# Performance work log

Hardware: AMD Instinct MI355X
Metric: run time of the kernel (lower is better)

The kernel has to match this reference:

```python
import jax, jax.numpy as jnp
import numpy as np

N = 4096   # nodes
E = 4096   # hyperedges (== N so the original's [N,H] output is fully populated)
F = 256    # feature_size
H = 256    # hidden_size
BLOCK = 64 # node-block size for the blocked masked max/min scan


def setup_inputs() -> dict:
    key = jax.random.key(0)
    ks = jax.random.split(key, 11)
    mask = jax.random.randint(ks[4], (E, N), 0, 2, dtype=jnp.int32)
    # guarantee every hyperedge is non-empty (matches `if end > start` path)
    mask = mask.at[jnp.arange(E), jnp.arange(N)].set(1)
    s = 0.05
    return {
        "pos_features": jax.random.normal(ks[0], (N, F), jnp.float32),
        "pos_matrix": jax.random.normal(ks[1], (N, F), jnp.float32),
        "neg_features": jax.random.normal(ks[2], (N, F), jnp.float32),
        "neg_matrix": jax.random.normal(ks[3], (N, F), jnp.float32),
        "batch_mask": mask,
        "W_self": jax.random.normal(ks[5], (F, H), jnp.float32) * s,
        "b_self": jnp.zeros((H,), jnp.float32),
        "W_hyper": jax.random.normal(ks[6], (F, H), jnp.float32) * s,
        "b_hyper": jnp.zeros((H,), jnp.float32),
        "W_score": jax.random.normal(ks[7], (H, 1), jnp.float32) * s,
        "b_score": jnp.zeros((1,), jnp.float32),
    }


def maxmin_pool(mask_bool, feats):
    """Per-hyperedge (max - min) over member-node features.
    mask_bool: [E, N] bool, feats: [N, H] -> [E, H].
    Blocked over nodes to avoid materializing [E, N, H]."""
    Ee, Nn = mask_bool.shape
    Hh = feats.shape[1]
    nb = Nn // BLOCK
    mask_blocks = mask_bool.reshape(Ee, nb, BLOCK).transpose(1, 0, 2)  # [nb, E, BLOCK]
    feat_blocks = feats.reshape(nb, BLOCK, Hh)                          # [nb, BLOCK, H]

    def body(carry, xs):
        mx, mn = carry
        mblk, fblk = xs                      # [E, BLOCK], [BLOCK, H]
        m = mblk[:, :, None]                 # [E, BLOCK, 1]
        f = fblk[None]                       # [1, BLOCK, H]
        mx = jnp.maximum(mx, jnp.max(jnp.where(m, f, -jnp.inf), axis=1))
        mn = jnp.minimum(mn, jnp.min(jnp.where(m, f, jnp.inf), axis=1))
        return (mx, mn), None

    init = (jnp.full((Ee, Hh), -jnp.inf, feats.dtype),
            jnp.full((Ee, Hh), jnp.inf, feats.dtype))
    (mx, mn), _ = jax.lax.scan(body, init, (mask_blocks, feat_blocks))
    return mx - mn


def reference(pos_features, pos_matrix, neg_features, neg_matrix, batch_mask,
              W_self, b_self, W_hyper, b_hyper, W_score, b_score):
    mask = batch_mask.astype(bool)

    def branch(x_feat, x_mat):
        h = jax.nn.relu(x_feat @ W_self + b_self + x_mat @ W_hyper + b_hyper)  # [N, H]
        pooled = maxmin_pool(mask, h)                                          # [E, H]
        return jax.nn.sigmoid(pooled @ W_score + b_score)                      # [E, 1]

    pos_score = branch(pos_features, pos_matrix)
    neg_score = branch(neg_features, neg_matrix)
    return pos_score, neg_score
```

## Files before the change

kernel.cpp:

```cpp
#include <hip/hip_runtime.h>
#include <hip/hip_bf16.h>
#include <hip/hip_fp16.h>


typedef short bf16x8 __attribute__((ext_vector_type(8)));
typedef float f32x4 __attribute__((ext_vector_type(4)));
typedef short s16x2 __attribute__((ext_vector_type(2)));
typedef unsigned short u16x2 __attribute__((ext_vector_type(2)));

static __device__ __forceinline__ unsigned short f2bf(float f) {
    __hip_bfloat16 b = __float2bfloat16(f);
    return __builtin_bit_cast(unsigned short, b);
}
static __device__ __forceinline__ float f16u_to_f(unsigned u) {
    __half h = __builtin_bit_cast(__half, (unsigned short)(u & 0xffffu));
    return __half2float(h);
}
static __device__ __forceinline__ unsigned pkmax_i16(unsigned a, unsigned b) {
    s16x2 r = __builtin_elementwise_max(__builtin_bit_cast(s16x2, a), __builtin_bit_cast(s16x2, b));
    return __builtin_bit_cast(unsigned, r);
}
static __device__ __forceinline__ unsigned pkmin_u16(unsigned a, unsigned b) {
    u16x2 r = __builtin_elementwise_min(__builtin_bit_cast(u16x2, a), __builtin_bit_cast(u16x2, b));
    return __builtin_bit_cast(unsigned, r);
}

__global__ void k_prepW(const float* __restrict__ Ws, const float* __restrict__ Wh,
                        unsigned short* __restrict__ Wts, unsigned short* __restrict__ Wth) {
    __shared__ unsigned short tile[64][65];
    const int k0 = blockIdx.x * 64, n0 = blockIdx.y * 64;
    const float* W     = blockIdx.z ? Wh : Ws;
    unsigned short* Wt = blockIdx.z ? Wth : Wts;
    const int t = threadIdx.x;
#pragma unroll
    for (int m = 0; m < 16; m++) {
        int li = t + m * 256; int r = li >> 6, c = li & 63;
        tile[r][c] = f2bf(W[(size_t)(k0 + r) * 256 + n0 + c]);
    }
    __syncthreads();
#pragma unroll
    for (int m = 0; m < 16; m++) {
        int li = t + m * 256; int c2 = li >> 6, r2 = li & 63;
        Wt[(size_t)(n0 + c2) * 256 + k0 + r2] = tile[r2][c2];
    }
}

__global__ void k_pack(const int* __restrict__ mask, unsigned* __restrict__ packed) {
    const int w = blockIdx.x * 256 + threadIdx.x;
    const int* p = mask + (size_t)w * 32;
    unsigned word = 0;
#pragma unroll
    for (int j = 0; j < 32; j += 4) {
        int4 m = *(const int4*)(p + j);
        word |= (m.x != 0 ? (1u << (31 - j)) : 0u)
              | (m.y != 0 ? (1u << (30 - j)) : 0u)
              | (m.z != 0 ? (1u << (29 - j)) : 0u)
              | (m.w != 0 ? (1u << (28 - j)) : 0u);
    }
    packed[w] = word;
}

__launch_bounds__(256)
__global__ void k_gemm_relu(const float* __restrict__ pXf, const float* __restrict__ pXm,
                            const float* __restrict__ nXf, const float* __restrict__ nXm,
                            const unsigned short* __restrict__ Wts, const unsigned short* __restrict__ Wth,
                            const float* __restrict__ bs,  const float* __restrict__ bh,
                            unsigned short* __restrict__ hOut, int tmode) {
    const int t  = threadIdx.x;
    const int wv = t >> 6;
    const int l  = t & 63;
    const int lm = l & 15;
    const int q  = l >> 4;
    const int bz = blockIdx.z;
    const float* Xf = bz ? nXf : pXf;
    const float* Xm = bz ? nXm : pXm;
    unsigned short* hb = hOut + (size_t)bz * 4096 * 256;

    const int m0 = blockIdx.x * 64 + wv * 16;
    const int n0 = blockIdx.y * 64;

    f32x4 acc[4] = {};
#pragma unroll
    for (int ks = 0; ks < 512; ks += 32) {
        const float* X           = (ks < 256) ? Xf : Xm;
        const unsigned short* Wt = (ks < 256) ? Wts : Wth;
        const int kk = (ks & 255) + q * 8;
        float4 a0 = *(const float4*)(X + (m0 + lm) * 256 + kk);
        float4 a1 = *(const float4*)(X + (m0 + lm) * 256 + kk + 4);
        bf16x8 a;
        a[0] = (short)f2bf(a0.x); a[1] = (short)f2bf(a0.y);
        a[2] = (short)f2bf(a0.z); a[3] = (short)f2bf(a0.w);
        a[4] = (short)f2bf(a1.x); a[5] = (short)f2bf(a1.y);
        a[6] = (short)f2bf(a1.z); a[7] = (short)f2bf(a1.w);
#pragma unroll
        for (int nt = 0; nt < 4; nt++) {
            bf16x8 b = *(const bf16x8*)(Wt + (n0 + nt * 16 + lm) * 256 + kk);
            acc[nt] = __builtin_amdgcn_mfma_f32_16x16x32_bf16(a, b, acc[nt], 0, 0, 0);
        }
    }
    if (tmode) {
#pragma unroll
        for (int nt = 0; nt < 4; nt++) {
            const int c = n0 + nt * 16 + lm;
            const float bsum = bs[c] + bh[c];
            ushort4 v4;
#pragma unroll
            for (int i = 0; i < 4; i++) {
                float v = acc[nt][i] + bsum;
                v = v > 0.f ? v : 0.f;
                ((unsigned short*)&v4)[i] = __builtin_bit_cast(unsigned short, __float2half(v));
            }
            *(ushort4*)(hb + (size_t)c * 4096 + m0 + q * 4) = v4;
        }
    } else {
#pragma unroll
        for (int nt = 0; nt < 4; nt++) {
            const int c = n0 + nt * 16 + lm;
            const float bsum = bs[c] + bh[c];
#pragma unroll
            for (int i = 0; i < 4; i++) {
                const int r = m0 + q * 4 + i;
                float v = acc[nt][i] + bsum;
                v = v > 0.f ? v : 0.f;
                hb[(size_t)r * 256 + c] = __builtin_bit_cast(unsigned short, __float2half(v));
            }
        }
    }
}

__launch_bounds__(256)
__global__ void k_sortpack(const unsigned short* __restrict__ hT,
                           const int* __restrict__ mask,
                           unsigned* __restrict__ packed,
                           unsigned* __restrict__ topkG, unsigned* __restrict__ botkG) {
    __shared__ unsigned arrA[4096];
    __shared__ unsigned arrB[4096];
    __shared__ unsigned short hist[16 * 256];

    const int c = blockIdx.x, br = blockIdx.y, t = threadIdx.x;
    const int wv = t >> 6, l = t & 63;
    const unsigned short* src = hT + (size_t)(br * 256 + c) * 4096;

    const int gtid = (br * 256 + c) * 256 + t;
    const int4* mp = (const int4*)(mask + (size_t)gtid * 128);
    int4 mr[16];
#pragma unroll
    for (int i = 0; i < 16; i++) mr[i] = mp[i];

    {
        uint4 a = ((const uint4*)src)[t * 2];
        uint4 b = ((const uint4*)src)[t * 2 + 1];
        unsigned base = t * 16;
        unsigned w[8] = {a.x, a.y, a.z, a.w, b.x, b.y, b.z, b.w};
#pragma unroll
        for (int m = 0; m < 8; m++) {
            arrA[base + 2 * m]     = ((w[m] & 0xFFFFu) << 16) | (base + 2 * m);
            arrA[base + 2 * m + 1] = (w[m] & 0xFFFF0000u)     | (base + 2 * m + 1);
        }
    }
    __syncthreads();

    unsigned pw[4];
#pragma unroll
    for (int m = 0; m < 2; m++) {
        unsigned word = 0;
#pragma unroll
        for (int j2 = 0; j2 < 8; j2++) {
            int4 v = mr[m * 8 + j2];
            const int j = j2 * 4;
            word |= (v.x != 0 ? (1u << (31 - j)) : 0u)
                  | (v.y != 0 ? (1u << (30 - j)) : 0u)
                  | (v.z != 0 ? (1u << (29 - j)) : 0u)
                  | (v.w != 0 ? (1u << (28 - j)) : 0u);
        }
        pw[m] = word;
    }
#pragma unroll
    for (int i = 0; i < 16; i++) mr[i] = mp[16 + i];

    unsigned* A = arrA;
    unsigned* B = arrB;
    auto do_pass = [&](int sh) {
        unsigned keys[16];
        unsigned short cnt[16];
#pragma unroll
        for (int b = 0; b < 16; b++) cnt[b] = 0;
#pragma unroll
        for (int m = 0; m < 16; m++) {
            keys[m] = A[t * 16 + m];
            cnt[(keys[m] >> sh) & 15u]++;
        }
#pragma unroll
        for (int b = 0; b < 16; b++) hist[b * 256 + t] = cnt[b];
        __syncthreads();

        unsigned loc[16];
        unsigned sum = 0;
#pragma unroll
        for (int m = 0; m < 16; m++) { loc[m] = sum; sum += hist[t * 16 + m]; }
        unsigned ws = sum;
#pragma unroll
        for (int off = 1; off < 64; off <<= 1) {
            unsigned n = __shfl_up(ws, off);
            if (l >= off) ws += n;
        }
        if (l == 63) B[wv] = ws;
        __syncthreads();
        unsigned wbase = 0;
#pragma unroll
        for (int w2 = 0; w2 < 4; w2++) if (w2 < wv) wbase += B[w2];
        const unsigned ex = wbase + ws - sum;
#pragma unroll
        for (int m = 0; m < 16; m++) hist[t * 16 + m] = (unsigned short)(ex + loc[m]);
        __syncthreads();

        unsigned offs[16];
#pragma unroll
        for (int b = 0; b < 16; b++) offs[b] = hist[b * 256 + t];
#pragma unroll
        for (int m = 0; m < 16; m++) {
            unsigned b = (keys[m] >> sh) & 15u;
            B[offs[b]++] = keys[m];
        }
        __syncthreads();
        unsigned* tmp = A; A = B; B = tmp;
    };

    do_pass(16);
#pragma unroll
    for (int m = 0; m < 2; m++) {
        unsigned word = 0;
#pragma unroll
        for (int j2 = 0; j2 < 8; j2++) {
            int4 v = mr[m * 8 + j2];
            const int j = j2 * 4;
            word |= (v.x != 0 ? (1u << (31 - j)) : 0u)
                  | (v.y != 0 ? (1u << (30 - j)) : 0u)
                  | (v.z != 0 ? (1u << (29 - j)) : 0u)
                  | (v.w != 0 ? (1u << (28 - j)) : 0u);
        }
        pw[2 + m] = word;
    }
    do_pass(20);
    do_pass(24);
    do_pass(28);

    if (t < 64) {
        topkG[(br * 64 + t) * 256 + c] = arrA[4095 - t];
        botkG[(br * 64 + t) * 256 + c] = arrA[t];
    }
    *(uint4*)(packed + (size_t)gtid * 4) = make_uint4(pw[0], pw[1], pw[2], pw[3]);
}

__launch_bounds__(256)
__global__ void k_probe(const unsigned* __restrict__ topkG,
                        const unsigned* __restrict__ botkG,
                        const unsigned* __restrict__ packed,
                        const unsigned short* __restrict__ hT,
                        const float* __restrict__ Wscore,
                        const float* __restrict__ bscore,
                        float* __restrict__ out) {
    __shared__ __align__(16) unsigned topkL[16 * 256];
    __shared__ __align__(16) unsigned botkL[16 * 256];
    __shared__ __align__(16) unsigned bitsL[16 * 128];

    const int t  = threadIdx.x;
    const int wv = t >> 6;
    const int l  = t & 63;
    const int e0 = blockIdx.x * 16;
    const int br = blockIdx.y;

    {
        const uint4* ts  = (const uint4*)(topkG + br * 16384);
        const uint4* bs2 = (const uint4*)(botkG + br * 16384);
#pragma unroll
        for (int m = 0; m < 4; m++) {
            ((uint4*)topkL)[t + m * 256] = ts[t + m * 256];
            ((uint4*)botkL)[t + m * 256] = bs2[t + m * 256];
        }
        ((uint4*)bitsL)[t]       = ((const uint4*)(packed + e0 * 128))[t];
        ((uint4*)bitsL)[t + 256] = ((const uint4*)(packed + e0 * 128))[t + 256];
    }
    __syncthreads();

    const float bsc = *bscore;
    float wsv[4];
#pragma unroll
    for (int sl = 0; sl < 4; sl++) wsv[sl] = Wscore[l + 64 * sl];

#pragma unroll 1
    for (int k = 0; k < 4; k++) {
        const int e = wv * 4 + k;
        const unsigned* mk = &bitsL[e * 128];
        float s = 0.f;
#pragma unroll
        for (int sl = 0; sl < 4; sl++) {
            const int c = l + 64 * sl;

            unsigned sel = 0xFFFFFFFFu;
#pragma unroll 1
            for (int g = 0; g < 2; g++) {
                unsigned kk[8]; int ss[8];
#pragma unroll
                for (int j = 0; j < 8; j++) kk[j] = topkL[(g * 8 + j) * 256 + c];
#pragma unroll
                for (int j = 0; j < 8; j++)
                    ss[j] = (int)(mk[(kk[j] & 4095u) >> 5] << (kk[j] & 31u));
                unsigned fnd = 0xFFFFFFFFu;
#pragma unroll
                for (int j = 7; j >= 0; j--) if (ss[j] < 0) fnd = kk[j];
                if (fnd != 0xFFFFFFFFu) { sel = fnd; break; }
            }
            if (sel == 0xFFFFFFFFu) {
                const unsigned* tg = topkG + br * 16384 + c;
#pragma unroll 1
                for (int p = 16; p < 64; p++) {
                    unsigned key = tg[p * 256];
                    if ((int)(mk[(key & 4095u) >> 5] << (key & 31u)) < 0) { sel = key; break; }
                }
            }
            if (sel == 0xFFFFFFFFu) {
                const unsigned short* col = hT + (size_t)(br * 256 + c) * 4096;
                unsigned best = 0;
#pragma unroll 1
                for (int n = 0; n < 4096; n++)
                    if ((int)(mk[n >> 5] << (n & 31)) < 0) { unsigned v = col[n]; if (v > best) best = v; }
                sel = best << 16;
            }
            const float vmax = f16u_to_f(sel >> 16);

            sel = 0xFFFFFFFFu;
#pragma unroll 1
            for (int g = 0; g < 2; g++) {
                unsigned kk[8]; int ss[8];
#pragma unroll
                for (int j = 0; j < 8; j++) kk[j] = botkL[(g * 8 + j) * 256 + c];
#pragma unroll
                for (int j = 0; j < 8; j++)
                    ss[j] = (int)(mk[(kk[j] & 4095u) >> 5] << (kk[j] & 31u));
                unsigned fnd = 0xFFFFFFFFu;
#pragma unroll
                for (int j = 7; j >= 0; j--) if (ss[j] < 0) fnd = kk[j];
                if (fnd != 0xFFFFFFFFu) { sel = fnd; break; }
            }
            if (sel == 0xFFFFFFFFu) {
                const unsigned* bg = botkG + br * 16384 + c;
#pragma unroll 1
                for (int p = 16; p < 64; p++) {
                    unsigned key = bg[p * 256];
                    if ((int)(mk[(key & 4095u) >> 5] << (key & 31u)) < 0) { sel = key; break; }
                }
            }
            if (sel == 0xFFFFFFFFu) {
                const unsigned short* col = hT + (size_t)(br * 256 + c) * 4096;
                unsigned best = 0xFFFFu;
#pragma unroll 1
                for (int n = 0; n < 4096; n++)
                    if ((int)(mk[n >> 5] << (n & 31)) < 0) { unsigned v = col[n]; if (v < best) best = v; }
                sel = best << 16;
            }
            const float vmin = f16u_to_f(sel >> 16);

            s += (vmax - vmin) * wsv[sl];
        }
#pragma unroll
        for (int off = 32; off; off >>= 1) s += __shfl_xor(s, off);
        if (l == 0)
            out[br * 4096 + e0 + e] = 1.f / (1.f + __expf(-(s + bsc)));
    }
}

#define POOL_STEP(WE, MX0, MX1, MN0, MN1, VX, VY)                          \
    {                                                                      \
        asm("s_add_u32 %[we], %[we], %[we]\n\t"                            \
            "s_cbranch_scc0 Lskip%=\n\t"                                   \
            "v_pk_max_i16 %[mx0], %[mx0], %[vx]\n\t"                       \
            "v_pk_max_i16 %[mx1], %[mx1], %[vy]\n\t"                       \
            "v_pk_min_u16 %[mn0], %[mn0], %[vx]\n\t"                       \
            "v_pk_min_u16 %[mn1], %[mn1], %[vy]\n"                         \
            "Lskip%=:"                                                     \
            : [we] "+s"(WE),                                               \
              [mx0] "+v"(MX0), [mx1] "+v"(MX1),                            \
              [mn0] "+v"(MN0), [mn1] "+v"(MN1)                             \
            : [vx] "v"(VX), [vy] "v"(VY)                                   \
            : "scc");                                                      \
    }

__launch_bounds__(512, 8)
__global__ void k_pool9(const unsigned short* __restrict__ hAll,
                        const unsigned* __restrict__ packed,
                        const float* __restrict__ Wscore,
                        const float* __restrict__ bscore,
                        float* __restrict__ out) {
    __shared__ __align__(16) unsigned bits[4 * 128];
    __shared__ __align__(16) unsigned part[8][4][64][4];

    const int t  = threadIdx.x;
    const int wv = t >> 6;
    const int l  = t & 63;
    const int e0 = blockIdx.x * 4;
    const int br = blockIdx.y;
    const unsigned short* h = hAll + (size_t)br * 4096 * 256;

    if (t < 128) ((uint4*)bits)[t] = ((const uint4*)(packed + e0 * 128))[t];
    __syncthreads();

    unsigned mx0[4], mx1[4], mn0[4], mn1[4];
#pragma unroll
    for (int e = 0; e < 4; e++) {
        mx0[e] = 0x80008000u; mx1[e] = 0x80008000u;
        mn0[e] = 0xFFFFFFFFu; mn1[e] = 0xFFFFFFFFu;
    }

#pragma unroll 1
    for (int ch = 0; ch < 16; ch++) {
        const int w0 = wv * 16 + ch;
        unsigned we0 = (unsigned)__builtin_amdgcn_readfirstlane((int)bits[0 * 128 + w0]);
        unsigned we1 = (unsigned)__builtin_amdgcn_readfirstlane((int)bits[1 * 128 + w0]);
        unsigned we2 = (unsigned)__builtin_amdgcn_readfirstlane((int)bits[2 * 128 + w0]);
        unsigned we3 = (unsigned)__builtin_amdgcn_readfirstlane((int)bits[3 * 128 + w0]);

        const unsigned short* hp = h + (size_t)(wv * 512 + ch * 32) * 256 + 4 * l;
#pragma unroll
        for (int jj = 0; jj < 8; jj++) {
            uint2 v0 = *(const uint2*)(hp + (jj * 4 + 0) * 256);
            uint2 v1 = *(const uint2*)(hp + (jj * 4 + 1) * 256);
            uint2 v2 = *(const uint2*)(hp + (jj * 4 + 2) * 256);
            uint2 v3 = *(const uint2*)(hp + (jj * 4 + 3) * 256);

            POOL_STEP(we0, mx0[0], mx1[0], mn0[0], mn1[0], v0.x, v0.y);
            POOL_STEP(we1, mx0[1], mx1[1], mn0[1], mn1[1], v0.x, v0.y);
            POOL_STEP(we2, mx0[2], mx1[2], mn0[2], mn1[2], v0.x, v0.y);
            POOL_STEP(we3, mx0[3], mx1[3], mn0[3], mn1[3], v0.x, v0.y);
            POOL_STEP(we0, mx0[0], mx1[0], mn0[0], mn1[0], v1.x, v1.y);
            POOL_STEP(we1, mx0[1], mx1[1], mn0[1], mn1[1], v1.x, v1.y);
            POOL_STEP(we2, mx0[2], mx1[2], mn0[2], mn1[2], v1.x, v1.y);
            POOL_STEP(we3, mx0[3], mx1[3], mn0[3], mn1[3], v1.x, v1.y);
            POOL_STEP(we0, mx0[0], mx1[0], mn0[0], mn1[0], v2.x, v2.y);
            POOL_STEP(we1, mx0[1], mx1[1], mn0[1], mn1[1], v2.x, v2.y);
            POOL_STEP(we2, mx0[2], mx1[2], mn0[2], mn1[2], v2.x, v2.y);
            POOL_STEP(we3, mx0[3], mx1[3], mn0[3], mn1[3], v2.x, v2.y);
            POOL_STEP(we0, mx0[0], mx1[0], mn0[0], mn1[0], v3.x, v3.y);
            POOL_STEP(we1, mx0[1], mx1[1], mn0[1], mn1[1], v3.x, v3.y);
            POOL_STEP(we2, mx0[2], mx1[2], mn0[2], mn1[2], v3.x, v3.y);
            POOL_STEP(we3, mx0[3], mx1[3], mn0[3], mn1[3], v3.x, v3.y);
        }
    }

#pragma unroll
    for (int e = 0; e < 4; e++) {
        uint4 p; p.x = mx0[e]; p.y = mx1[e]; p.z = mn0[e]; p.w = mn1[e];
        *(uint4*)&part[wv][e][l][0] = p;
    }
    __syncthreads();

    if (wv < 4) {
        unsigned rmx0 = 0x80008000u, rmx1 = 0x80008000u;
        unsigned rmn0 = 0xFFFFFFFFu, rmn1 = 0xFFFFFFFFu;
#pragma unroll
        for (int w2 = 0; w2 < 8; w2++) {
            uint4 p = *(const uint4*)&part[w2][wv][l][0];
            rmx0 = pkmax_i16(rmx0, p.x);  rmx1 = pkmax_i16(rmx1, p.y);
            rmn0 = pkmin_u16(rmn0, p.z);  rmn1 = pkmin_u16(rmn1, p.w);
        }
        float4 wsv = *(const float4*)(Wscore + 4 * l);
        const float bsc = *bscore;
        float s = (f16u_to_f(rmx0)       - f16u_to_f(rmn0))       * wsv.x
                + (f16u_to_f(rmx0 >> 16) - f16u_to_f(rmn0 >> 16)) * wsv.y
                + (f16u_to_f(rmx1)       - f16u_to_f(rmn1))       * wsv.z
                + (f16u_to_f(rmx1 >> 16) - f16u_to_f(rmn1 >> 16)) * wsv.w;
#pragma unroll
        for (int off = 32; off; off >>= 1) s += __shfl_xor(s, off);
        if (l == 0)
            out[br * 4096 + e0 + wv] = 1.f / (1.f + __expf(-(s + bsc)));
    }
}

extern "C" void kernel_launch(void* const* d_in, const int* in_sizes, int n_in,
                              void* d_out, int out_size, void* d_ws, size_t ws_size,
                              hipStream_t stream) {
    const float* pf  = (const float*)d_in[0];
    const float* pm  = (const float*)d_in[1];
    const float* nf  = (const float*)d_in[2];
    const float* nm  = (const float*)d_in[3];
    const int*   msk = (const int*)d_in[4];
    const float* Wsf = (const float*)d_in[5];
    const float* bsf = (const float*)d_in[6];
    const float* Whp = (const float*)d_in[7];
    const float* bhp = (const float*)d_in[8];
    const float* Wsc = (const float*)d_in[9];
    const float* bsc = (const float*)d_in[10];
    float* out = (float*)d_out;

    char* ws = (char*)d_ws;
    const size_t MB = 1024u * 1024u;
    unsigned short* hbuf  = (unsigned short*)(ws);
    unsigned*       pck   = (unsigned*)(ws + 4 * MB);
    unsigned short* Wts   = (unsigned short*)(ws + 6 * MB);
    unsigned short* Wth   = Wts + 256 * 256;
    unsigned*       topkG = (unsigned*)(ws + 6 * MB + 256 * 1024);
    unsigned*       botkG = (unsigned*)(ws + 6 * MB + 384 * 1024);
    const size_t need = 6 * MB + 512 * 1024;

    k_prepW<<<dim3(4, 4, 2), 256, 0, stream>>>(Wsf, Whp, Wts, Wth);

    if (ws_size >= need) {
        k_gemm_relu<<<dim3(64, 4, 2), 256, 0, stream>>>(pf, pm, nf, nm, Wts, Wth, bsf, bhp, hbuf, 1);
        k_sortpack<<<dim3(256, 2), 256, 0, stream>>>(hbuf, msk, pck, topkG, botkG);
        k_probe<<<dim3(256, 2), 256, 0, stream>>>(topkG, botkG, pck, hbuf, Wsc, bsc, out);
    } else {
        k_pack<<<2048, 256, 0, stream>>>(msk, pck);
        k_gemm_relu<<<dim3(64, 4, 2), 256, 0, stream>>>(pf, pm, nf, nm, Wts, Wth, bsf, bhp, hbuf, 0);
        k_pool9<<<dim3(1024, 2), 512, 0, stream>>>(hbuf, pck, Wsc, bsc, out);
    }
}
```

Measured before the change: 188.6 us.

## Double sortpack threads and pad LDS to cut bank conflicts in radix sort

Rebuilds the per-column radix-sort-and-pack kernel to use 512 threads with 8 keys each instead of 256 threads with 16. Keys stay in registers across passes, the per-thread digit histogram is built with packed nibble counters, and the in-thread rank is found with a small prior-match count instead of incrementing offsets. LDS indices are padded to reduce bank conflicts. Each thread packs half as much mask data, which raises parallelism and lowers per-thread register and serial work, at the cost of more LDS and larger scan and synchronisation groups.

After: 175.1 us. 7.2% less time.

```diff
diff --git a/kernel.cpp b/kernel.cpp
--- a/kernel.cpp
+++ b/kernel.cpp
@@ -24,6 +24,8 @@
     u16x2 r = __builtin_elementwise_min(__builtin_bit_cast(u16x2, a), __builtin_bit_cast(u16x2, b));
     return __builtin_bit_cast(unsigned, r);
 }
+static __device__ __forceinline__ int fpad(int i) { return i + (i >> 4); }
+static __device__ __forceinline__ int fh(int i)   { return i + (i >> 3); }
 
 __global__ void k_prepW(const float* __restrict__ Ws, const float* __restrict__ Wh,
                         unsigned short* __restrict__ Wts, unsigned short* __restrict__ Wth) {
@@ -128,128 +130,118 @@
     }
 }
 
-__launch_bounds__(256)
+__launch_bounds__(512)
 __global__ void k_sortpack(const unsigned short* __restrict__ hT,
                            const int* __restrict__ mask,
                            unsigned* __restrict__ packed,
                            unsigned* __restrict__ topkG, unsigned* __restrict__ botkG) {
-    __shared__ unsigned arrA[4096];
-    __shared__ unsigned arrB[4096];
-    __shared__ unsigned short hist[16 * 256];
+    __shared__ unsigned arrA[4352];
+    __shared__ unsigned arrB[4352];
+    __shared__ unsigned short hist[9216];
 
     const int c = blockIdx.x, br = blockIdx.y, t = threadIdx.x;
     const int wv = t >> 6, l = t & 63;
     const unsigned short* src = hT + (size_t)(br * 256 + c) * 4096;
 
-    const int gtid = (br * 256 + c) * 256 + t;
-    const int4* mp = (const int4*)(mask + (size_t)gtid * 128);
-    int4 mr[16];
-#pragma unroll
-    for (int i = 0; i < 16; i++) mr[i] = mp[i];
-
+    const int gt = (br * 256 + c) * 512 + t;
+    const int4* mp = (const int4*)(mask + (size_t)gt * 64);
+    int4 mr[8];
+#pragma unroll
+    for (int i = 0; i < 8; i++) mr[i] = mp[i];
+
+    unsigned keys[8];
     {
-        uint4 a = ((const uint4*)src)[t * 2];
-        uint4 b = ((const uint4*)src)[t * 2 + 1];
-        unsigned base = t * 16;
-        unsigned w[8] = {a.x, a.y, a.z, a.w, b.x, b.y, b.z, b.w};
-#pragma unroll
-        for (int m = 0; m < 8; m++) {
-            arrA[base + 2 * m]     = ((w[m] & 0xFFFFu) << 16) | (base + 2 * m);
-            arrA[base + 2 * m + 1] = (w[m] & 0xFFFF0000u)     | (base + 2 * m + 1);
-        }
-    }
-    __syncthreads();
-
-    unsigned pw[4];
-#pragma unroll
-    for (int m = 0; m < 2; m++) {
+        uint4 a = ((const uint4*)src)[t];
+        unsigned base = t * 8;
+        unsigned w[4] = {a.x, a.y, a.z, a.w};
+#pragma unroll
+        for (int m = 0; m < 4; m++) {
+            keys[2 * m]     = ((w[m] & 0xFFFFu) << 16) | (base + 2 * m);
+            keys[2 * m + 1] = (w[m] & 0xFFFF0000u)     | (base + 2 * m + 1);
+        }
+    }
+
+    auto cvt = [&]() -> unsigned {
         unsigned word = 0;
 #pragma unroll
         for (int j2 = 0; j2 < 8; j2++) {
-            int4 v = mr[m * 8 + j2];
+            int4 v = mr[j2];
             const int j = j2 * 4;
             word |= (v.x != 0 ? (1u << (31 - j)) : 0u)
                   | (v.y != 0 ? (1u << (30 - j)) : 0u)
                   | (v.z != 0 ? (1u << (29 - j)) : 0u)
                   | (v.w != 0 ? (1u << (28 - j)) : 0u);
         }
-        pw[m] = word;
-    }
-#pragma unroll
-    for (int i = 0; i < 16; i++) mr[i] = mp[16 + i];
-
-    unsigned* A = arrA;
-    unsigned* B = arrB;
-    auto do_pass = [&](int sh) {
-        unsigned keys[16];
-        unsigned short cnt[16];
-#pragma unroll
-        for (int b = 0; b < 16; b++) cnt[b] = 0;
-#pragma unroll
-        for (int m = 0; m < 16; m++) {
-            keys[m] = A[t * 16 + m];
-            cnt[(keys[m] >> sh) & 15u]++;
-        }
-#pragma unroll
-        for (int b = 0; b < 16; b++) hist[b * 256 + t] = cnt[b];
+        return word;
+    };
+
+    auto sort_pass = [&](int sh, unsigned* Bp) {
+        unsigned d[8];
+        unsigned c0 = 0, c1 = 0;
+#pragma unroll
+        for (int m = 0; m < 8; m++) {
+            d[m] = (keys[m] >> sh) & 15u;
+            unsigned inc = 1u << ((d[m] & 7u) * 4);
+            if (d[m] < 8u) c0 += inc; else c1 += inc;
+        }
+#pragma unroll
+        for (int b = 0; b < 8; b++) hist[fh(b * 512 + t)]       = (unsigned short)((c0 >> (b * 4)) & 15u);
+#pragma unroll
+        for (int b = 0; b < 8; b++) hist[fh((b + 8) * 512 + t)] = (unsigned short)((c1 >> (b * 4)) & 15u);
         __syncthreads();
 
         unsigned loc[16];
         unsigned sum = 0;
 #pragma unroll
-        for (int m = 0; m < 16; m++) { loc[m] = sum; sum += hist[t * 16 + m]; }
+        for (int m = 0; m < 16; m++) { loc[m] = sum; sum += hist[fh(t * 16 + m)]; }
         unsigned ws = sum;
 #pragma unroll
         for (int off = 1; off < 64; off <<= 1) {
             unsigned n = __shfl_up(ws, off);
             if (l >= off) ws += n;
         }
-        if (l == 63) B[wv] = ws;
+        if (l == 63) Bp[wv] = ws;
         __syncthreads();
         unsigned wbase = 0;
 #pragma unroll
-        for (int w2 = 0; w2 < 4; w2++) if (w2 < wv) wbase += B[w2];
+        for (int w2 = 0; w2 < 8; w2++) if (w2 < wv) wbase += Bp[w2];
         const unsigned ex = wbase + ws - sum;
 #pragma unroll
-        for (int m = 0; m < 16; m++) hist[t * 16 + m] = (unsigned short)(ex + loc[m]);
+        for (int m = 0; m < 16; m++) hist[fh(t * 16 + m)] = (unsigned short)(ex + loc[m]);
         __syncthreads();
 
-        unsigned offs[16];
-#pragma unroll
-        for (int b = 0; b < 16; b++) offs[b] = hist[b * 256 + t];
-#pragma unroll
-        for (int m = 0; m < 16; m++) {
-            unsigned b = (keys[m] >> sh) & 15u;
-            B[offs[b]++] = keys[m];
+#pragma unroll
+        for (int m = 0; m < 8; m++) {
+            unsigned rank = hist[fh((int)d[m] * 512 + t)];
+            unsigned prior = 0;
+#pragma unroll
+            for (int j = 0; j < m; j++) prior += (d[j] == d[m]) ? 1u : 0u;
+            Bp[fpad((int)(rank + prior))] = keys[m];
         }
         __syncthreads();
-        unsigned* tmp = A; A = B; B = tmp;
     };
 
-    do_pass(16);
-#pragma unroll
-    for (int m = 0; m < 2; m++) {
-        unsigned word = 0;
-#pragma unroll
-        for (int j2 = 0; j2 < 8; j2++) {
-            int4 v = mr[m * 8 + j2];
-            const int j = j2 * 4;
-            word |= (v.x != 0 ? (1u << (31 - j)) : 0u)
-                  | (v.y != 0 ? (1u << (30 - j)) : 0u)
-                  | (v.z != 0 ? (1u << (29 - j)) : 0u)
-                  | (v.w != 0 ? (1u << (28 - j)) : 0u);
-        }
-        pw[2 + m] = word;
-    }
-    do_pass(20);
-    do_pass(24);
-    do_pass(28);
+    auto load_keys = [&](const unsigned* Ap) {
+        const unsigned* ap = Ap + t * 8 + (t >> 1);
+#pragma unroll
+        for (int m = 0; m < 8; m++) keys[m] = ap[m];
+    };
+
+    const unsigned pw0 = cvt();
+#pragma unroll
+    for (int i = 0; i < 8; i++) mr[i] = mp[8 + i];
+
+    sort_pass(16, arrB);
+    const unsigned pw1 = cvt();
+    load_keys(arrB); sort_pass(20, arrA);
+    load_keys(arrA); sort_pass(24, arrB);
+    load_keys(arrB); sort_pass(28, arrA);
 
     if (t < 64) {
-        topkG[(br * 64 + t) * 256 + c] = arrA[4095 - t];
-        botkG[(br * 64 + t) * 256 + c] = arrA[t];
-    }
-    *(uint4*)(packed + (size_t)gtid * 4) = make_uint4(pw[0], pw[1], pw[2], pw[3]);
+        topkG[(br * 64 + t) * 256 + c] = arrA[fpad(4095 - t)];
+        botkG[(br * 64 + t) * 256 + c] = arrA[fpad(t)];
+    }
+    *(uint2*)(packed + (size_t)gt * 2) = make_uint2(pw0, pw1);
 }
 
 __launch_bounds__(256)
@@ -506,7 +498,7 @@
 
     if (ws_size >= need) {
         k_gemm_relu<<<dim3(64, 4, 2), 256, 0, stream>>>(pf, pm, nf, nm, Wts, Wth, bsf, bhp, hbuf, 1);
-        k_sortpack<<<dim3(256, 2), 256, 0, stream>>>(hbuf, msk, pck, topkG, botkG);
+        k_sortpack<<<dim3(256, 2), 512, 0, stream>>>(hbuf, msk, pck, topkG, botkG);
         k_probe<<<dim3(256, 2), 256, 0, stream>>>(topkG, botkG, pck, hbuf, Wsc, bsc, out);
     } else {
         k_pack<<<2048, 256, 0, stream>>>(msk, pck);
```
